# Performance work log

Measured on AMD Instinct MI355X. Metric: run time of the kernel, lower is better.

## Reference

```python
import jax, jax.numpy as jnp
import numpy as np

REG_WEIGHT = 1e-4
N_LAYERS = 3


def setup_inputs() -> dict:
    key = jax.random.key(0)
    ks = jax.random.split(key, 7)
    n_users, n_items, d = 100000, 50000, 64
    E, B = 1600000, 4096
    return {
        "user_table": jax.random.normal(ks[0], (n_users, d), dtype=jnp.float32) * 0.01,
        "item_table": jax.random.normal(ks[1], (n_items, d), dtype=jnp.float32) * 0.01,
        "edge_u": jax.random.randint(ks[2], (E,), 0, n_users, dtype=jnp.int32),
        "edge_i": jax.random.randint(ks[3], (E,), 0, n_items, dtype=jnp.int32),
        "users": jax.random.randint(ks[4], (B,), 0, n_users, dtype=jnp.int32),
        "pos_items": jax.random.randint(ks[5], (B,), 0, n_items, dtype=jnp.int32),
        "neg_items": jax.random.randint(ks[6], (B,), 0, n_items, dtype=jnp.int32),
    }


def _lightgcn_embeddings(user_table, item_table, edge_u, edge_i):
    n_users, n_items = user_table.shape[0], item_table.shape[0]
    N = n_users + n_items
    E = edge_u.shape[0]
    ones = jnp.ones((E,), dtype=user_table.dtype)
    # symmetric normalization D^{-1/2} A D^{-1/2} on the bipartite graph
    deg_u = jax.ops.segment_sum(ones, edge_u, num_segments=n_users)
    deg_i = jax.ops.segment_sum(ones, edge_i, num_segments=n_items)
    w = jax.lax.rsqrt(jnp.maximum(deg_u[edge_u] * deg_i[edge_i], 1.0))
    # symmetric edge list over the stacked [users; items] node set
    rows = jnp.concatenate([edge_u, edge_i + n_users])
    cols = jnp.concatenate([edge_i + n_users, edge_u])
    vals = jnp.concatenate([w, w])[:, None]

    x = jnp.concatenate([user_table, item_table], axis=0)  # [N, d]
    acc = x
    for _ in range(N_LAYERS):
        x = jax.ops.segment_sum(x[cols] * vals, rows, num_segments=N)
        acc = acc + x
    final = acc / jnp.asarray(N_LAYERS + 1, dtype=x.dtype)
    return final[:n_users], final[n_users:]


def reference(user_table, item_table, edge_u, edge_i, users, pos_items, neg_items):
    user_emb_all, item_emb_all = _lightgcn_embeddings(user_table, item_table, edge_u, edge_i)
    u_emb = user_emb_all[users]
    pos_i_emb = item_emb_all[pos_items]
    neg_i_emb = item_emb_all[neg_items]
    pos_scores = jnp.sum(u_emb * pos_i_emb, axis=-1)
    neg_scores = jnp.sum(u_emb * neg_i_emb, axis=-1)
    # L2 regularization on the layer-0 (table) embeddings
    u0 = user_table[users]
    p0 = item_table[pos_items]
    n0 = item_table[neg_items]
    reg_loss = REG_WEIGHT * (jnp.sum(u0 * u0) + jnp.sum(p0 * p0) + jnp.sum(n0 * n0))
    reg_loss = reg_loss / users.shape[0]
    return pos_scores, neg_scores, reg_loss
```

## Files before the change

kernel.cpp:

```cpp
#include <hip/hip_runtime.h>
#include <hip/hip_fp16.h>

#define THREADS 256
#define BIN_C 4096
#define NBMAX 400
#define CAP 4608
#define SH_U 8
#define SH_I 7
#define CPAD 16
#define T_TILES 8
#define TSH_U 13
#define TSH_I 14

__global__ void bin_kernel(const int* __restrict__ eu, const int* __restrict__ ei,
                           int* __restrict__ bcnt_u, int* __restrict__ bcnt_i,
                           int* __restrict__ binu, int* __restrict__ bini,
                           int E, int nbu, int nbi) {
    __shared__ int hist_u[NBMAX], hist_i[NBMAX];
    __shared__ int base_u[NBMAX], base_i[NBMAX];
    int tid = threadIdx.x;
    int e0 = blockIdx.x * BIN_C;
    if (e0 >= E) return;
    int cnt = min(BIN_C, E - e0);

    for (int b = tid; b < NBMAX; b += THREADS) { hist_u[b] = 0; hist_i[b] = 0; }
    __syncthreads();

    int u[16], v[16];
    #pragma unroll
    for (int j = 0; j < 16; ++j) {
        int k = tid + j * THREADS;
        if (k < cnt) { u[j] = eu[e0 + k]; v[j] = ei[e0 + k]; }
        else         { u[j] = -1; v[j] = -1; }
    }
    #pragma unroll
    for (int j = 0; j < 16; ++j) {
        if (u[j] >= 0) {
            atomicAdd(&hist_u[u[j] >> SH_U], 1);
            atomicAdd(&hist_i[v[j] >> SH_I], 1);
        }
    }
    __syncthreads();
    for (int b = tid; b < NBMAX; b += THREADS) {
        int cu = hist_u[b], ci = hist_i[b];
        base_u[b] = (cu > 0 && b < nbu) ? atomicAdd(&bcnt_u[(size_t)b * CPAD], cu) : 0;
        base_i[b] = (ci > 0 && b < nbi) ? atomicAdd(&bcnt_i[(size_t)b * CPAD], ci) : 0;
        hist_u[b] = 0; hist_i[b] = 0;
    }
    __syncthreads();
    #pragma unroll
    for (int j = 0; j < 16; ++j) {
        if (u[j] >= 0) {
            int bu = u[j] >> SH_U;
            int pu = base_u[bu] + atomicAdd(&hist_u[bu], 1);
            if (pu < CAP) binu[(size_t)bu * CAP + pu] = ((u[j] & 255) << 16) | v[j];
            int bi = v[j] >> SH_I;
            int pi = base_i[bi] + atomicAdd(&hist_i[bi], 1);
            if (pi < CAP) bini[(size_t)bi * CAP + pi] = ((v[j] & 127) << 17) | u[j];
        }
    }
}

__global__ void place(const int* __restrict__ bcnt_u, const int* __restrict__ bcnt_i,
                      const int* __restrict__ binu, const int* __restrict__ bini,
                      int* __restrict__ offu, int* __restrict__ offi,
                      int* __restrict__ du, int* __restrict__ di,
                      float* __restrict__ rsdu, float* __restrict__ rsdi,
                      int* __restrict__ entu, int* __restrict__ enti,
                      int* __restrict__ curs,
                      int nbu, int nU, int nI) {
    __shared__ int stash[CAP];
    __shared__ int bin_cnt[THREADS * T_TILES];
    __shared__ int node_base[THREADS];
    __shared__ int wsum[4];
    __shared__ int bob_sh;
    int b = blockIdx.x;
    bool isU = (b < nbu);
    const int* bin; int base_node, nn, count;
    int *off, *deg, *ent; float* rsd;
    int losh, tsh, lomask;
    if (isU) {
        bin = binu + (size_t)b * CAP;
        base_node = b << SH_U; nn = min(256, nU - base_node);
        count = min(bcnt_u[(size_t)b * CPAD], CAP);
        off = offu; deg = du; rsd = rsdu; ent = entu;
        losh = 16; tsh = TSH_U; lomask = 0xFFFF;
    } else {
        int b2 = b - nbu;
        bin = bini + (size_t)b2 * CAP;
        base_node = b2 << SH_I; nn = min(128, nI - base_node);
        count = min(bcnt_i[(size_t)b2 * CPAD], CAP);
        off = offi; deg = di; rsd = rsdi; ent = enti;
        losh = 17; tsh = TSH_I; lomask = 0x1FFFF;
    }
    int tid = threadIdx.x;
    #pragma unroll
    for (int t = 0; t < T_TILES; ++t) bin_cnt[tid + t * THREADS] = 0;
    __syncthreads();
    for (int k = tid; k < count; k += THREADS) {
        int p = bin[k];
        stash[k] = p;
        int key = ((p >> losh) << 3) | ((p & lomask) >> tsh);
        atomicAdd(&bin_cnt[key], 1);
    }
    __syncthreads();
    int c = 0;
    {
        int base = tid * T_TILES;
        #pragma unroll
        for (int t = 0; t < T_TILES; ++t) {
            int v = bin_cnt[base + t];
            bin_cnt[base + t] = c;
            c += v;
        }
    }
    int seg = (c + 15) & ~15;
    int lane = tid & 63, wid = tid >> 6;
    int inc = seg;
    #pragma unroll
    for (int ofs = 1; ofs < 64; ofs <<= 1) {
        int t = __shfl_up(inc, ofs);
        if (lane >= ofs) inc += t;
    }
    if (lane == 63) wsum[wid] = inc;
    __syncthreads();
    int wofs = 0;
    #pragma unroll
    for (int w = 0; w < 4; ++w) wofs += (w < wid) ? wsum[w] : 0;
    int incl = inc + wofs;
    int excl = incl - seg;
    if (tid == THREADS - 1) bob_sh = atomicAdd(&curs[isU ? 0 : 1], incl);
    __syncthreads();
    int bob = bob_sh;
    node_base[tid] = excl;
    if (tid < nn) {
        off[base_node + tid] = bob + excl;
        deg[base_node + tid] = c;
        rsd[base_node + tid] = rsqrtf(fmaxf((float)c, 1.0f));
    }
    __syncthreads();
    #pragma unroll
    for (int t = 0; t < T_TILES; ++t) {
        int k = tid + t * THREADS;
        bin_cnt[k] += node_base[k >> 3];
    }
    __syncthreads();
    for (int k = tid; k < count; k += THREADS) {
        int p = stash[k];
        int key = ((p >> losh) << 3) | ((p & lomask) >> tsh);
        int sl = atomicAdd(&bin_cnt[key], 1);
        ent[bob + sl] = p & lomask;
    }
}

__global__ void conv16all(const float* __restrict__ ut, const float* __restrict__ it,
                          __half* __restrict__ dst, int nU16, int ntot16) {
    int stride = gridDim.x * blockDim.x;
    for (int i = blockIdx.x * blockDim.x + threadIdx.x; i < ntot16; i += stride) {
        const float* src = (i < nU16) ? (ut + (size_t)i * 4) : (it + (size_t)(i - nU16) * 4);
        float4 v = *reinterpret_cast<const float4*>(src);
        __half2 h0 = __float22half2_rn(make_float2(v.x, v.y));
        __half2 h1 = __float22half2_rn(make_float2(v.z, v.w));
        uint2 st;
        st.x = *reinterpret_cast<unsigned*>(&h0);
        st.y = *reinterpret_cast<unsigned*>(&h1);
        *reinterpret_cast<uint2*>(dst + (size_t)i * 4) = st;
    }
}

__global__ void prop16(const __half* __restrict__ x,
                       const int* __restrict__ offu, const int* __restrict__ offi,
                       const int* __restrict__ du, const int* __restrict__ di,
                       const float* __restrict__ rsdu, const float* __restrict__ rsdi,
                       const int* __restrict__ entu, const int* __restrict__ enti,
                       __half* __restrict__ y, int nU, int N) {
    int node = blockIdx.x * (THREADS >> 3) + (threadIdx.x >> 3);
    int lane = threadIdx.x & 7;
    if (node >= N) return;
    const int* ent; const __half* src; const float* rsdn;
    int beg, dg; float rs;
    if (node < nU) {
        beg = offu[node]; dg = du[node]; rs = rsdu[node];
        ent = entu; src = x + ((size_t)nU << 6); rsdn = rsdi;
    } else {
        int i = node - nU;
        beg = offi[i]; dg = di[i]; rs = rsdi[i];
        ent = enti; src = x; rsdn = rsdu;
    }
    float a0=0,a1=0,a2=0,a3=0,a4=0,a5=0,a6=0,a7=0;
    for (int k0 = 0; k0 < dg; k0 += 8) {
        int me = (k0 + lane < dg) ? ent[beg + k0 + lane] : 0;
        #pragma unroll
        for (int j = 0; j < 8; ++j) {
            if (k0 + j < dg) {
                int nbr = __shfl(me, j, 8);
                float w = rsdn[nbr];
                uint4 r = *reinterpret_cast<const uint4*>(src + ((size_t)nbr << 6) + (lane << 3));
                __half2 h0 = *reinterpret_cast<__half2*>(&r.x);
                __half2 h1 = *reinterpret_cast<__half2*>(&r.y);
                __half2 h2 = *reinterpret_cast<__half2*>(&r.z);
                __half2 h3 = *reinterpret_cast<__half2*>(&r.w);
                float2 f0 = __half22float2(h0), f1 = __half22float2(h1);
                float2 f2 = __half22float2(h2), f3 = __half22float2(h3);
                a0 += w * f0.x; a1 += w * f0.y; a2 += w * f1.x; a3 += w * f1.y;
                a4 += w * f2.x; a5 += w * f2.y; a6 += w * f3.x; a7 += w * f3.y;
            }
        }
    }
    __half2 o0 = __float22half2_rn(make_float2(a0 * rs, a1 * rs));
    __half2 o1 = __float22half2_rn(make_float2(a2 * rs, a3 * rs));
    __half2 o2 = __float22half2_rn(make_float2(a4 * rs, a5 * rs));
    __half2 o3 = __float22half2_rn(make_float2(a6 * rs, a7 * rs));
    uint4 st;
    st.x = *reinterpret_cast<unsigned*>(&o0);
    st.y = *reinterpret_cast<unsigned*>(&o1);
    st.z = *reinterpret_cast<unsigned*>(&o2);
    st.w = *reinterpret_cast<unsigned*>(&o3);
    *reinterpret_cast<uint4*>(y + ((size_t)node << 6) + (lane << 3)) = st;
}

__global__ void prop_sel_acc(const __half* __restrict__ x,
                             const int* __restrict__ users, const int* __restrict__ pos,
                             const int* __restrict__ neg,
                             const int* __restrict__ offu, const int* __restrict__ offi,
                             const int* __restrict__ du, const int* __restrict__ di,
                             const float* __restrict__ rsdu, const float* __restrict__ rsdi,
                             const int* __restrict__ entu, const int* __restrict__ enti,
                             float* __restrict__ sel, int B, int nU) {
    int r = blockIdx.x * (THREADS >> 3) + (threadIdx.x >> 3);
    int lane = threadIdx.x & 7;
    if (r >= 3 * B) return;
    int which = r / B, b = r - which * B;
    const int* ent; const __half* src; const float* rsdn;
    int beg, dg; float rs; size_t selfrow;
    if (which == 0) {
        int u = users[b];
        beg = offu[u]; dg = du[u]; rs = rsdu[u];
        ent = entu; src = x + ((size_t)nU << 6); rsdn = rsdi;
        selfrow = (size_t)u << 6;
    } else {
        int i = (which == 1) ? pos[b] : neg[b];
        beg = offi[i]; dg = di[i]; rs = rsdi[i];
        ent = enti; src = x; rsdn = rsdu;
        selfrow = (size_t)(nU + i) << 6;
    }
    float a0=0,a1=0,a2=0,a3=0,a4=0,a5=0,a6=0,a7=0;
    for (int k0 = 0; k0 < dg; k0 += 8) {
        int me = (k0 + lane < dg) ? ent[beg + k0 + lane] : 0;
        #pragma unroll
        for (int j = 0; j < 8; ++j) {
            if (k0 + j < dg) {
                int nbr = __shfl(me, j, 8);
                float w = rsdn[nbr];
                uint4 rv = *reinterpret_cast<const uint4*>(src + ((size_t)nbr << 6) + (lane << 3));
                __half2 h0 = *reinterpret_cast<__half2*>(&rv.x);
                __half2 h1 = *reinterpret_cast<__half2*>(&rv.y);
                __half2 h2 = *reinterpret_cast<__half2*>(&rv.z);
                __half2 h3 = *reinterpret_cast<__half2*>(&rv.w);
                float2 f0 = __half22float2(h0), f1 = __half22float2(h1);
                float2 f2 = __half22float2(h2), f3 = __half22float2(h3);
                a0 += w * f0.x; a1 += w * f0.y; a2 += w * f1.x; a3 += w * f1.y;
                a4 += w * f2.x; a5 += w * f2.y; a6 += w * f3.x; a7 += w * f3.y;
            }
        }
    }
    uint4 rv = *reinterpret_cast<const uint4*>(x + selfrow + (lane << 3));
    __half2 h0 = *reinterpret_cast<__half2*>(&rv.x);
    __half2 h1 = *reinterpret_cast<__half2*>(&rv.y);
    __half2 h2 = *reinterpret_cast<__half2*>(&rv.z);
    __half2 h3 = *reinterpret_cast<__half2*>(&rv.w);
    float2 s0 = __half22float2(h0), s1 = __half22float2(h1);
    float2 s2 = __half22float2(h2), s3 = __half22float2(h3);
    float* s = sel + ((size_t)r << 6) + (lane << 3);
    float4 d0 = *reinterpret_cast<float4*>(s);
    float4 d1 = *reinterpret_cast<float4*>(s + 4);
    d0.x += s0.x + rs * a0; d0.y += s0.y + rs * a1;
    d0.z += s1.x + rs * a2; d0.w += s1.y + rs * a3;
    d1.x += s2.x + rs * a4; d1.y += s2.y + rs * a5;
    d1.z += s3.x + rs * a6; d1.w += s3.y + rs * a7;
    *reinterpret_cast<float4*>(s) = d0;
    *reinterpret_cast<float4*>(s + 4) = d1;
}

__global__ void selreg(const float* __restrict__ ut, const float* __restrict__ it,
                       const int* __restrict__ users, const int* __restrict__ pos,
                       const int* __restrict__ neg,
                       float* __restrict__ sel, float* __restrict__ out_reg,
                       int B, float scale) {
    int r = blockIdx.x * (THREADS >> 4) + (threadIdx.x >> 4);
    int t = threadIdx.x & 15;
    float ssq = 0.f;
    if (r < 3 * B) {
        int which = r / B, b = r - which * B;
        const float* base; int idx;
        if (which == 0)      { base = ut; idx = users[b]; }
        else if (which == 1) { base = it; idx = pos[b]; }
        else                 { base = it; idx = neg[b]; }
        float4 v = *reinterpret_cast<const float4*>(base + ((size_t)idx << 6) + t * 4);
        *reinterpret_cast<float4*>(sel + ((size_t)r << 6) + t * 4) = v;
        ssq = v.x * v.x + v.y * v.y + v.z * v.z + v.w * v.w;
    }
    #pragma unroll
    for (int ofs = 32; ofs; ofs >>= 1) ssq += __shfl_down(ssq, ofs);
    if ((threadIdx.x & 63) == 0) atomicAdd(out_reg, ssq * scale);
}

__global__ void sel_acc16(const __half* __restrict__ x,
                          const int* __restrict__ users, const int* __restrict__ pos,
                          const int* __restrict__ neg, float* __restrict__ sel, int B, int nU) {
    int r = blockIdx.x * (THREADS >> 3) + (threadIdx.x >> 3);
    int lane = threadIdx.x & 7;
    if (r >= 3 * B) return;
    int which = r / B, b = r - which * B;
    size_t row;
    if (which == 0)      row = (size_t)users[b];
    else if (which == 1) row = (size_t)nU + pos[b];
    else                 row = (size_t)nU + neg[b];
    uint4 rv = *reinterpret_cast<const uint4*>(x + (row << 6) + (lane << 3));
    __half2 h0 = *reinterpret_cast<__half2*>(&rv.x);
    __half2 h1 = *reinterpret_cast<__half2*>(&rv.y);
    __half2 h2 = *reinterpret_cast<__half2*>(&rv.z);
    __half2 h3 = *reinterpret_cast<__half2*>(&rv.w);
    float2 f0 = __half22float2(h0), f1 = __half22float2(h1);
    float2 f2 = __half22float2(h2), f3 = __half22float2(h3);
    float* s = sel + ((size_t)r << 6) + (lane << 3);
    float4 d0 = *reinterpret_cast<float4*>(s);
    float4 d1 = *reinterpret_cast<float4*>(s + 4);
    d0.x += f0.x; d0.y += f0.y; d0.z += f1.x; d0.w += f1.y;
    d1.x += f2.x; d1.y += f2.y; d1.z += f3.x; d1.w += f3.y;
    *reinterpret_cast<float4*>(s) = d0;
    *reinterpret_cast<float4*>(s + 4) = d1;
}

__global__ void score(const float* __restrict__ sel, float* __restrict__ out, int B) {
    int b = blockIdx.x * (THREADS >> 6) + (threadIdx.x >> 6);
    int lane = threadIdx.x & 63;
    if (b >= B) return;
    float u = sel[((size_t)b << 6) + lane];
    float p = sel[((size_t)(B + b) << 6) + lane];
    float n = sel[((size_t)(2 * B + b) << 6) + lane];
    float ps = u * p, ns = u * n;
    for (int ofs = 32; ofs; ofs >>= 1) {
        ps += __shfl_down(ps, ofs);
        ns += __shfl_down(ns, ofs);
    }
    if (lane == 0) {
        out[b]     = ps * (1.0f / 16.0f);
        out[B + b] = ns * (1.0f / 16.0f);
    }
}

extern "C" void kernel_launch(void* const* d_in, const int* in_sizes, int n_in,
                              void* d_out, int out_size, void* d_ws, size_t ws_size,
                              hipStream_t stream) {
    const float* ut   = (const float*)d_in[0];
    const float* it   = (const float*)d_in[1];
    const int* eu     = (const int*)d_in[2];
    const int* ei     = (const int*)d_in[3];
    const int* users  = (const int*)d_in[4];
    const int* pos    = (const int*)d_in[5];
    const int* neg    = (const int*)d_in[6];
    int nU = in_sizes[0] / 64;
    int nI = in_sizes[1] / 64;
    int E  = in_sizes[2];
    int B  = in_sizes[4];
    int N  = nU + nI;
    float* out = (float*)d_out;

    int nbu = (nU + 255) >> SH_U;
    int nbi = (nI + 127) >> SH_I;

    char* ws = (char*)d_ws;
    size_t cursor = 0;
    auto alloc = [&](size_t bytes) -> void* {
        cursor = (cursor + 255) & ~(size_t)255;
        void* p = ws + cursor;
        cursor += bytes;
        return p;
    };
    int*   bcnt_u = (int*)alloc((size_t)nbu * CPAD * 4);
    int*   bcnt_i = (int*)alloc((size_t)nbi * CPAD * 4);
    int*   curs   = (int*)alloc(2 * 4);
    size_t zero_span = cursor;
    int*   binu = (int*)alloc((size_t)nbu * CAP * 4);
    int*   bini = (int*)alloc((size_t)nbi * CAP * 4);
    int*   offu = (int*)alloc((size_t)nU * 4);
    int*   offi = (int*)alloc((size_t)nI * 4);
    int*   du   = (int*)alloc((size_t)nU * 4);
    int*   di   = (int*)alloc((size_t)nI * 4);
    float* rsdu = (float*)alloc((size_t)nU * 4);
    float* rsdi = (float*)alloc((size_t)nI * 4);
    int*   entu = (int*)alloc(((size_t)E + (size_t)nbu * 256 * 16) * 4);
    int*   enti = (int*)alloc(((size_t)E + (size_t)nbi * 128 * 16) * 4);
    __half* xA  = (__half*)alloc((size_t)N * 64 * 2);
    __half* xB  = (__half*)alloc((size_t)N * 64 * 2);
    float* sel  = (float*)alloc((size_t)3 * B * 64 * 4);

    hipMemsetAsync(d_ws, 0, zero_span, stream);
    hipMemsetAsync(out + 2 * B, 0, sizeof(float), stream);

    conv16all<<<2048, THREADS, 0, stream>>>(ut, it, xA, nU * 16, N * 16);

    int nchunks = (E + BIN_C - 1) / BIN_C;
    bin_kernel<<<nchunks, THREADS, 0, stream>>>(eu, ei, bcnt_u, bcnt_i, binu, bini, E, nbu, nbi);
    place<<<nbu + nbi, THREADS, 0, stream>>>(bcnt_u, bcnt_i, binu, bini,
                                             offu, offi, du, di, rsdu, rsdi, entu, enti,
                                             curs, nbu, nU, nI);

    selreg<<<(3 * B + 15) / 16, THREADS, 0, stream>>>(ut, it, users, pos, neg, sel,
                                                      out + 2 * B, B, 1e-4f / (float)B);

    int gridSel16 = (3 * B * 8 + THREADS - 1) / THREADS;
    int gridProp = (N * 8 + THREADS - 1) / THREADS;
    prop16<<<gridProp, THREADS, 0, stream>>>(xA, offu, offi, du, di, rsdu, rsdi, entu, enti, xB, nU, N);
    sel_acc16<<<gridSel16, THREADS, 0, stream>>>(xB, users, pos, neg, sel, B, nU);
    prop16<<<gridProp, THREADS, 0, stream>>>(xB, offu, offi, du, di, rsdu, rsdi, entu, enti, xA, nU, N);
    prop_sel_acc<<<gridSel16, THREADS, 0, stream>>>(xA, users, pos, neg, offu, offi, du, di,
                                                    rsdu, rsdi, entu, enti, sel, B, nU);

    score<<<(B + 3) / 4, THREADS, 0, stream>>>(sel, out, B);
}
```

Baseline: 284.7 us.

## Replace global-atomic edge binning with per-chunk local sort and offset tables

The binning kernel no longer reserves space in global per-bin counters with atomics. Each chunk now sorts its edges by bin into its own contiguous region and writes a per-chunk prefix table. The place kernel then gathers each bin's slices from every chunk via these tables. This removes contended global atomics and scattered writes, but place now reads about 391 small segments per bin with serial per-thread loops and uneven lengths.

```diff
diff --git a/kernel.cpp b/kernel.cpp
--- a/kernel.cpp
+++ b/kernel.cpp
@@ -2,8 +2,8 @@
 #include <hip/hip_fp16.h>
 
 #define THREADS 256
-#define BIN_C 4096
-#define NBMAX 400
+#define BIN_C2 4096
+#define NBMAX 392
 #define CAP 4608
 #define SH_U 8
 #define SH_I 7
@@ -12,94 +12,117 @@
 #define TSH_U 13
 #define TSH_I 14
 
-__global__ void bin_kernel(const int* __restrict__ eu, const int* __restrict__ ei,
-                           int* __restrict__ bcnt_u, int* __restrict__ bcnt_i,
-                           int* __restrict__ binu, int* __restrict__ bini,
-                           int E, int nbu, int nbi) {
-    __shared__ int hist_u[NBMAX], hist_i[NBMAX];
-    __shared__ int base_u[NBMAX], base_i[NBMAX];
+__global__ void binpack(const int* __restrict__ eu, const int* __restrict__ ei,
+                        int* __restrict__ regu, int* __restrict__ regi,
+                        int* __restrict__ sTu, int* __restrict__ sTi,
+                        int E, int nbu, int nbi) {
+    int c = blockIdx.x;
+    bool isU = (blockIdx.y == 0);
+    const int* key   = isU ? eu : ei;
+    const int* other = isU ? ei : eu;
+    int nb   = isU ? nbu : nbi;
+    int sh   = isU ? SH_U : SH_I;
+    int losh = isU ? 16 : 17;
+    int lomsk = (1 << sh) - 1;
+    int* reg = isU ? regu : regi;
+    int* sT  = (isU ? sTu : sTi) + (size_t)c * (NBMAX);
+    __shared__ int hist[NBMAX];
+    __shared__ int wsum[4];
     int tid = threadIdx.x;
-    int e0 = blockIdx.x * BIN_C;
-    if (e0 >= E) return;
-    int cnt = min(BIN_C, E - e0);
-
-    for (int b = tid; b < NBMAX; b += THREADS) { hist_u[b] = 0; hist_i[b] = 0; }
-    __syncthreads();
-
-    int u[16], v[16];
-    #pragma unroll
-    for (int j = 0; j < 16; ++j) {
-        int k = tid + j * THREADS;
-        if (k < cnt) { u[j] = eu[e0 + k]; v[j] = ei[e0 + k]; }
-        else         { u[j] = -1; v[j] = -1; }
-    }
-    #pragma unroll
-    for (int j = 0; j < 16; ++j) {
-        if (u[j] >= 0) {
-            atomicAdd(&hist_u[u[j] >> SH_U], 1);
-            atomicAdd(&hist_i[v[j] >> SH_I], 1);
-        }
-    }
-    __syncthreads();
-    for (int b = tid; b < NBMAX; b += THREADS) {
-        int cu = hist_u[b], ci = hist_i[b];
-        base_u[b] = (cu > 0 && b < nbu) ? atomicAdd(&bcnt_u[(size_t)b * CPAD], cu) : 0;
-        base_i[b] = (ci > 0 && b < nbi) ? atomicAdd(&bcnt_i[(size_t)b * CPAD], ci) : 0;
-        hist_u[b] = 0; hist_i[b] = 0;
-    }
-    __syncthreads();
-    #pragma unroll
-    for (int j = 0; j < 16; ++j) {
-        if (u[j] >= 0) {
-            int bu = u[j] >> SH_U;
-            int pu = base_u[bu] + atomicAdd(&hist_u[bu], 1);
-            if (pu < CAP) binu[(size_t)bu * CAP + pu] = ((u[j] & 255) << 16) | v[j];
-            int bi = v[j] >> SH_I;
-            int pi = base_i[bi] + atomicAdd(&hist_i[bi], 1);
-            if (pi < CAP) bini[(size_t)bi * CAP + pi] = ((v[j] & 127) << 17) | u[j];
-        }
-    }
-}
-
-__global__ void place(const int* __restrict__ bcnt_u, const int* __restrict__ bcnt_i,
-                      const int* __restrict__ binu, const int* __restrict__ bini,
+    int e0 = c * BIN_C2;
+    int cnt = min(BIN_C2, E - e0);
+    if (cnt <= 0) return;
+    for (int b = tid; b < nb; b += THREADS) hist[b] = 0;
+    __syncthreads();
+    for (int k = tid; k < cnt; k += THREADS)
+        atomicAdd(&hist[key[e0 + k] >> sh], 1);
+    __syncthreads();
+    int b0 = tid * 2;
+    int v0 = (b0 < nb)     ? hist[b0]     : 0;
+    int v1 = (b0 + 1 < nb) ? hist[b0 + 1] : 0;
+    int s2 = v0 + v1;
+    int lane = tid & 63, wid = tid >> 6;
+    int inc = s2;
+    #pragma unroll
+    for (int ofs = 1; ofs < 64; ofs <<= 1) {
+        int t = __shfl_up(inc, ofs);
+        if (lane >= ofs) inc += t;
+    }
+    if (lane == 63) wsum[wid] = inc;
+    __syncthreads();
+    int wofs = 0;
+    #pragma unroll
+    for (int w = 0; w < 4; ++w) wofs += (w < wid) ? wsum[w] : 0;
+    int excl = inc - s2 + wofs;
+    __syncthreads();
+    if (b0 < nb)     { hist[b0] = excl;          sT[b0] = excl; }
+    if (b0 + 1 < nb) { hist[b0 + 1] = excl + v0; sT[b0 + 1] = excl + v0; }
+    if (tid == THREADS - 1) sT[nb] = cnt;
+    __syncthreads();
+    for (int k = tid; k < cnt; k += THREADS) {
+        int kn = key[e0 + k];
+        int o  = other[e0 + k];
+        int b  = kn >> sh;
+        int p  = ((kn & lomsk) << losh) | o;
+        int pos = atomicAdd(&hist[b], 1);
+        reg[(size_t)c * BIN_C2 + pos] = p;
+    }
+}
+
+__global__ void place(const int* __restrict__ regu, const int* __restrict__ regi,
+                      const int* __restrict__ sTu, const int* __restrict__ sTi,
                       int* __restrict__ offu, int* __restrict__ offi,
                       int* __restrict__ du, int* __restrict__ di,
                       float* __restrict__ rsdu, float* __restrict__ rsdi,
                       int* __restrict__ entu, int* __restrict__ enti,
                       int* __restrict__ curs,
-                      int nbu, int nU, int nI) {
+                      int nbu, int nU, int nI, int nchunks) {
     __shared__ int stash[CAP];
     __shared__ int bin_cnt[THREADS * T_TILES];
     __shared__ int node_base[THREADS];
     __shared__ int wsum[4];
     __shared__ int bob_sh;
+    __shared__ int scursor;
     int b = blockIdx.x;
     bool isU = (b < nbu);
-    const int* bin; int base_node, nn, count;
+    int bidx = isU ? b : (b - nbu);
+    const int* reg = isU ? regu : regi;
+    const int* sT  = isU ? sTu : sTi;
+    int base_node, nn;
     int *off, *deg, *ent; float* rsd;
-    int losh, tsh, lomask;
+    int losh, tsh;
     if (isU) {
-        bin = binu + (size_t)b * CAP;
-        base_node = b << SH_U; nn = min(256, nU - base_node);
-        count = min(bcnt_u[(size_t)b * CPAD], CAP);
+        base_node = bidx << SH_U; nn = min(256, nU - base_node);
         off = offu; deg = du; rsd = rsdu; ent = entu;
-        losh = 16; tsh = TSH_U; lomask = 0xFFFF;
+        losh = 16; tsh = TSH_U;
     } else {
-        int b2 = b - nbu;
-        bin = bini + (size_t)b2 * CAP;
-        base_node = b2 << SH_I; nn = min(128, nI - base_node);
-        count = min(bcnt_i[(size_t)b2 * CPAD], CAP);
+        base_node = bidx << SH_I; nn = min(128, nI - base_node);
         off = offi; deg = di; rsd = rsdi; ent = enti;
-        losh = 17; tsh = TSH_I; lomask = 0x1FFFF;
-    }
+        losh = 17; tsh = TSH_I;
+    }
+    int lomask = (1 << losh) - 1;
     int tid = threadIdx.x;
+    if (tid == 0) scursor = 0;
     #pragma unroll
     for (int t = 0; t < T_TILES; ++t) bin_cnt[tid + t * THREADS] = 0;
     __syncthreads();
+    for (int c = tid; c < nchunks; c += THREADS) {
+        const int* row = sT + (size_t)c * NBMAX;
+        int s = row[bidx], e = row[bidx + 1];
+        int len = e - s;
+        if (len > 0) {
+            int base = atomicAdd(&scursor, len);
+            const int* src = reg + (size_t)c * BIN_C2 + s;
+            for (int j = 0; j < len; ++j) {
+                int pos = base + j;
+                if (pos < CAP) stash[pos] = src[j];
+            }
+        }
+    }
+    __syncthreads();
+    int count = min(scursor, CAP);
     for (int k = tid; k < count; k += THREADS) {
-        int p = bin[k];
-        stash[k] = p;
+        int p = stash[k];
         int key = ((p >> losh) << 3) | ((p & lomask) >> tsh);
         atomicAdd(&bin_cnt[key], 1);
     }
@@ -129,7 +152,7 @@
     for (int w = 0; w < 4; ++w) wofs += (w < wid) ? wsum[w] : 0;
     int incl = inc + wofs;
     int excl = incl - seg;
-    if (tid == THREADS - 1) bob_sh = atomicAdd(&curs[isU ? 0 : 1], incl);
+    if (tid == THREADS - 1) bob_sh = atomicAdd(&curs[isU ? 0 : CPAD], incl);
     __syncthreads();
     int bob = bob_sh;
     node_base[tid] = excl;
@@ -369,6 +392,7 @@
 
     int nbu = (nU + 255) >> SH_U;
     int nbi = (nI + 127) >> SH_I;
+    int nchunks = (E + BIN_C2 - 1) / BIN_C2;
 
     char* ws = (char*)d_ws;
     size_t cursor = 0;
@@ -378,12 +402,12 @@
         cursor += bytes;
         return p;
     };
-    int*   bcnt_u = (int*)alloc((size_t)nbu * CPAD * 4);
-    int*   bcnt_i = (int*)alloc((size_t)nbi * CPAD * 4);
-    int*   curs   = (int*)alloc(2 * 4);
+    int*   curs = (int*)alloc(2 * CPAD * 4);
     size_t zero_span = cursor;
-    int*   binu = (int*)alloc((size_t)nbu * CAP * 4);
-    int*   bini = (int*)alloc((size_t)nbi * CAP * 4);
+    int*   regu = (int*)alloc((size_t)nchunks * BIN_C2 * 4);
+    int*   regi = (int*)alloc((size_t)nchunks * BIN_C2 * 4);
+    int*   sTu  = (int*)alloc((size_t)nchunks * NBMAX * 4);
+    int*   sTi  = (int*)alloc((size_t)nchunks * NBMAX * 4);
     int*   offu = (int*)alloc((size_t)nU * 4);
     int*   offi = (int*)alloc((size_t)nI * 4);
     int*   du   = (int*)alloc((size_t)nU * 4);
@@ -401,11 +425,10 @@
 
     conv16all<<<2048, THREADS, 0, stream>>>(ut, it, xA, nU * 16, N * 16);
 
-    int nchunks = (E + BIN_C - 1) / BIN_C;
-    bin_kernel<<<nchunks, THREADS, 0, stream>>>(eu, ei, bcnt_u, bcnt_i, binu, bini, E, nbu, nbi);
-    place<<<nbu + nbi, THREADS, 0, stream>>>(bcnt_u, bcnt_i, binu, bini,
+    binpack<<<dim3(nchunks, 2), THREADS, 0, stream>>>(eu, ei, regu, regi, sTu, sTi, E, nbu, nbi);
+    place<<<nbu + nbi, THREADS, 0, stream>>>(regu, regi, sTu, sTi,
                                              offu, offi, du, di, rsdu, rsdi, entu, enti,
-                                             curs, nbu, nU, nI);
+                                             curs, nbu, nU, nI, nchunks);
 
     selreg<<<(3 * B + 15) / 16, THREADS, 0, stream>>>(ut, it, users, pos, neg, sel,
                                                       out + 2 * B, B, 1e-4f / (float)B);
```

Result: no change. 280.6 us (-1.4%).

## Merge independent kernels into multi-role launches and add nontemporal edge loads/stores

Applied to the files above, without the earlier changes.

Merges the fp16 conversion, edge binning and selection/regularization kernels into one launch that picks its role from blockIdx.y. It also folds the first layer's selection accumulation into the second propagation launch as extra blocks. Together these cut the launch count and let independent work overlap. Edge-list loads and propagation output stores now use nontemporal hints, and the place cursors are padded apart to avoid sharing a cache line. The risks are oversized grids with many idle blocks and poorer cache reuse of the nontemporal output, which the next layer reads back.

```diff
diff --git a/kernel.cpp b/kernel.cpp
--- a/kernel.cpp
+++ b/kernel.cpp
@@ -12,20 +12,61 @@
 #define TSH_U 13
 #define TSH_I 14
 
-__global__ void bin_kernel(const int* __restrict__ eu, const int* __restrict__ ei,
-                           int* __restrict__ bcnt_u, int* __restrict__ bcnt_i,
-                           int* __restrict__ binu, int* __restrict__ bini,
-                           int E, int nbu, int nbi) {
+typedef unsigned u32x4 __attribute__((ext_vector_type(4)));
+
+__global__ void megaA(const float* __restrict__ ut, const float* __restrict__ it,
+                      __half* __restrict__ dst, int nU16, int ntot16,
+                      const int* __restrict__ eu, const int* __restrict__ ei,
+                      int* __restrict__ bcnt_u, int* __restrict__ bcnt_i,
+                      int* __restrict__ binu, int* __restrict__ bini,
+                      int E, int nbu, int nbi, int nchunks,
+                      const int* __restrict__ users, const int* __restrict__ pos,
+                      const int* __restrict__ neg,
+                      float* __restrict__ sel, float* __restrict__ out_reg,
+                      int B, float scale) {
+    int tid = threadIdx.x;
+    if (blockIdx.y == 0) {
+        int stride = gridDim.x * blockDim.x;
+        for (int i = blockIdx.x * blockDim.x + tid; i < ntot16; i += stride) {
+            const float* src = (i < nU16) ? (ut + (size_t)i * 4) : (it + (size_t)(i - nU16) * 4);
+            float4 v = *reinterpret_cast<const float4*>(src);
+            __half2 h0 = __float22half2_rn(make_float2(v.x, v.y));
+            __half2 h1 = __float22half2_rn(make_float2(v.z, v.w));
+            uint2 st;
+            st.x = *reinterpret_cast<unsigned*>(&h0);
+            st.y = *reinterpret_cast<unsigned*>(&h1);
+            *reinterpret_cast<uint2*>(dst + (size_t)i * 4) = st;
+        }
+        return;
+    }
+    if (blockIdx.y == 2) {
+        int r = blockIdx.x * (THREADS >> 4) + (tid >> 4);
+        int t = tid & 15;
+        float ssq = 0.f;
+        if (r < 3 * B) {
+            int which = r / B, b = r - which * B;
+            const float* base; int idx;
+            if (which == 0)      { base = ut; idx = users[b]; }
+            else if (which == 1) { base = it; idx = pos[b]; }
+            else                 { base = it; idx = neg[b]; }
+            float4 v = *reinterpret_cast<const float4*>(base + ((size_t)idx << 6) + t * 4);
+            *reinterpret_cast<float4*>(sel + ((size_t)r << 6) + t * 4) = v;
+            ssq = v.x * v.x + v.y * v.y + v.z * v.z + v.w * v.w;
+        }
+        #pragma unroll
+        for (int ofs = 32; ofs; ofs >>= 1) ssq += __shfl_down(ssq, ofs);
+        if ((tid & 63) == 0) atomicAdd(out_reg, ssq * scale);
+        return;
+    }
     __shared__ int hist_u[NBMAX], hist_i[NBMAX];
     __shared__ int base_u[NBMAX], base_i[NBMAX];
-    int tid = threadIdx.x;
-    int e0 = blockIdx.x * BIN_C;
-    if (e0 >= E) return;
+    int c = blockIdx.x;
+    if (c >= nchunks) return;
+    int e0 = c * BIN_C;
     int cnt = min(BIN_C, E - e0);
-
+    if (cnt <= 0) return;
     for (int b = tid; b < NBMAX; b += THREADS) { hist_u[b] = 0; hist_i[b] = 0; }
     __syncthreads();
-
     int u[16], v[16];
     #pragma unroll
     for (int j = 0; j < 16; ++j) {
@@ -78,21 +119,22 @@
     bool isU = (b < nbu);
     const int* bin; int base_node, nn, count;
     int *off, *deg, *ent; float* rsd;
-    int losh, tsh, lomask;
+    int losh, tsh;
     if (isU) {
         bin = binu + (size_t)b * CAP;
         base_node = b << SH_U; nn = min(256, nU - base_node);
         count = min(bcnt_u[(size_t)b * CPAD], CAP);
         off = offu; deg = du; rsd = rsdu; ent = entu;
-        losh = 16; tsh = TSH_U; lomask = 0xFFFF;
+        losh = 16; tsh = TSH_U;
     } else {
         int b2 = b - nbu;
         bin = bini + (size_t)b2 * CAP;
         base_node = b2 << SH_I; nn = min(128, nI - base_node);
         count = min(bcnt_i[(size_t)b2 * CPAD], CAP);
         off = offi; deg = di; rsd = rsdi; ent = enti;
-        losh = 17; tsh = TSH_I; lomask = 0x1FFFF;
-    }
+        losh = 17; tsh = TSH_I;
+    }
+    int lomask = (1 << losh) - 1;
     int tid = threadIdx.x;
     #pragma unroll
     for (int t = 0; t < T_TILES; ++t) bin_cnt[tid + t * THREADS] = 0;
@@ -129,7 +171,7 @@
     for (int w = 0; w < 4; ++w) wofs += (w < wid) ? wsum[w] : 0;
     int incl = inc + wofs;
     int excl = incl - seg;
-    if (tid == THREADS - 1) bob_sh = atomicAdd(&curs[isU ? 0 : 1], incl);
+    if (tid == THREADS - 1) bob_sh = atomicAdd(&curs[isU ? 0 : CPAD], incl);
     __syncthreads();
     int bob = bob_sh;
     node_base[tid] = excl;
@@ -153,29 +195,12 @@
     }
 }
 
-__global__ void conv16all(const float* __restrict__ ut, const float* __restrict__ it,
-                          __half* __restrict__ dst, int nU16, int ntot16) {
-    int stride = gridDim.x * blockDim.x;
-    for (int i = blockIdx.x * blockDim.x + threadIdx.x; i < ntot16; i += stride) {
-        const float* src = (i < nU16) ? (ut + (size_t)i * 4) : (it + (size_t)(i - nU16) * 4);
-        float4 v = *reinterpret_cast<const float4*>(src);
-        __half2 h0 = __float22half2_rn(make_float2(v.x, v.y));
-        __half2 h1 = __float22half2_rn(make_float2(v.z, v.w));
-        uint2 st;
-        st.x = *reinterpret_cast<unsigned*>(&h0);
-        st.y = *reinterpret_cast<unsigned*>(&h1);
-        *reinterpret_cast<uint2*>(dst + (size_t)i * 4) = st;
-    }
-}
-
-__global__ void prop16(const __half* __restrict__ x,
-                       const int* __restrict__ offu, const int* __restrict__ offi,
-                       const int* __restrict__ du, const int* __restrict__ di,
-                       const float* __restrict__ rsdu, const float* __restrict__ rsdi,
-                       const int* __restrict__ entu, const int* __restrict__ enti,
-                       __half* __restrict__ y, int nU, int N) {
-    int node = blockIdx.x * (THREADS >> 3) + (threadIdx.x >> 3);
-    int lane = threadIdx.x & 7;
+__device__ __forceinline__ void prop_body(const __half* __restrict__ x,
+                                          const int* __restrict__ offu, const int* __restrict__ offi,
+                                          const int* __restrict__ du, const int* __restrict__ di,
+                                          const float* __restrict__ rsdu, const float* __restrict__ rsdi,
+                                          const int* __restrict__ entu, const int* __restrict__ enti,
+                                          __half* __restrict__ y, int nU, int N, int node, int lane) {
     if (node >= N) return;
     const int* ent; const __half* src; const float* rsdn;
     int beg, dg; float rs;
@@ -189,7 +214,7 @@
     }
     float a0=0,a1=0,a2=0,a3=0,a4=0,a5=0,a6=0,a7=0;
     for (int k0 = 0; k0 < dg; k0 += 8) {
-        int me = (k0 + lane < dg) ? ent[beg + k0 + lane] : 0;
+        int me = (k0 + lane < dg) ? __builtin_nontemporal_load(&ent[beg + k0 + lane]) : 0;
         #pragma unroll
         for (int j = 0; j < 8; ++j) {
             if (k0 + j < dg) {
@@ -211,12 +236,59 @@
     __half2 o1 = __float22half2_rn(make_float2(a2 * rs, a3 * rs));
     __half2 o2 = __float22half2_rn(make_float2(a4 * rs, a5 * rs));
     __half2 o3 = __float22half2_rn(make_float2(a6 * rs, a7 * rs));
-    uint4 st;
+    u32x4 st;
     st.x = *reinterpret_cast<unsigned*>(&o0);
     st.y = *reinterpret_cast<unsigned*>(&o1);
     st.z = *reinterpret_cast<unsigned*>(&o2);
     st.w = *reinterpret_cast<unsigned*>(&o3);
-    *reinterpret_cast<uint4*>(y + ((size_t)node << 6) + (lane << 3)) = st;
+    __builtin_nontemporal_store(st, reinterpret_cast<u32x4*>(y + ((size_t)node << 6) + (lane << 3)));
+}
+
+__global__ void prop16(const __half* __restrict__ x,
+                       const int* __restrict__ offu, const int* __restrict__ offi,
+                       const int* __restrict__ du, const int* __restrict__ di,
+                       const float* __restrict__ rsdu, const float* __restrict__ rsdi,
+                       const int* __restrict__ entu, const int* __restrict__ enti,
+                       __half* __restrict__ y, int nU, int N) {
+    int node = blockIdx.x * (THREADS >> 3) + (threadIdx.x >> 3);
+    prop_body(x, offu, offi, du, di, rsdu, rsdi, entu, enti, y, nU, N, node, threadIdx.x & 7);
+}
+
+__global__ void prop16_selacc(const __half* __restrict__ x,
+                              const int* __restrict__ offu, const int* __restrict__ offi,
+                              const int* __restrict__ du, const int* __restrict__ di,
+                              const float* __restrict__ rsdu, const float* __restrict__ rsdi,
+                              const int* __restrict__ entu, const int* __restrict__ enti,
+                              __half* __restrict__ y, int nU, int N, int gridProp,
+                              const int* __restrict__ users, const int* __restrict__ pos,
+                              const int* __restrict__ neg, float* __restrict__ sel, int B) {
+    int lane = threadIdx.x & 7;
+    if (blockIdx.x < gridProp) {
+        int node = blockIdx.x * (THREADS >> 3) + (threadIdx.x >> 3);
+        prop_body(x, offu, offi, du, di, rsdu, rsdi, entu, enti, y, nU, N, node, lane);
+        return;
+    }
+    int r = (blockIdx.x - gridProp) * (THREADS >> 3) + (threadIdx.x >> 3);
+    if (r >= 3 * B) return;
+    int which = r / B, b = r - which * B;
+    size_t row;
+    if (which == 0)      row = (size_t)users[b];
+    else if (which == 1) row = (size_t)nU + pos[b];
+    else                 row = (size_t)nU + neg[b];
+    uint4 rv = *reinterpret_cast<const uint4*>(x + (row << 6) + (lane << 3));
+    __half2 h0 = *reinterpret_cast<__half2*>(&rv.x);
+    __half2 h1 = *reinterpret_cast<__half2*>(&rv.y);
+    __half2 h2 = *reinterpret_cast<__half2*>(&rv.z);
+    __half2 h3 = *reinterpret_cast<__half2*>(&rv.w);
+    float2 f0 = __half22float2(h0), f1 = __half22float2(h1);
+    float2 f2 = __half22float2(h2), f3 = __half22float2(h3);
+    float* s = sel + ((size_t)r << 6) + (lane << 3);
+    float4 d0 = *reinterpret_cast<float4*>(s);
+    float4 d1 = *reinterpret_cast<float4*>(s + 4);
+    d0.x += f0.x; d0.y += f0.y; d0.z += f1.x; d0.w += f1.y;
+    d1.x += f2.x; d1.y += f2.y; d1.z += f3.x; d1.w += f3.y;
+    *reinterpret_cast<float4*>(s) = d0;
+    *reinterpret_cast<float4*>(s + 4) = d1;
 }
 
 __global__ void prop_sel_acc(const __half* __restrict__ x,
@@ -246,7 +318,7 @@
     }
     float a0=0,a1=0,a2=0,a3=0,a4=0,a5=0,a6=0,a7=0;
     for (int k0 = 0; k0 < dg; k0 += 8) {
-        int me = (k0 + lane < dg) ? ent[beg + k0 + lane] : 0;
+        int me = (k0 + lane < dg) ? __builtin_nontemporal_load(&ent[beg + k0 + lane]) : 0;
         #pragma unroll
         for (int j = 0; j < 8; ++j) {
             if (k0 + j < dg) {
@@ -282,56 +354,6 @@
     *reinterpret_cast<float4*>(s + 4) = d1;
 }
 
-__global__ void selreg(const float* __restrict__ ut, const float* __restrict__ it,
-                       const int* __restrict__ users, const int* __restrict__ pos,
-                       const int* __restrict__ neg,
-                       float* __restrict__ sel, float* __restrict__ out_reg,
-                       int B, float scale) {
-    int r = blockIdx.x * (THREADS >> 4) + (threadIdx.x >> 4);
-    int t = threadIdx.x & 15;
-    float ssq = 0.f;
-    if (r < 3 * B) {
-        int which = r / B, b = r - which * B;
-        const float* base; int idx;
-        if (which == 0)      { base = ut; idx = users[b]; }
-        else if (which == 1) { base = it; idx = pos[b]; }
-        else                 { base = it; idx = neg[b]; }
-        float4 v = *reinterpret_cast<const float4*>(base + ((size_t)idx << 6) + t * 4);
-        *reinterpret_cast<float4*>(sel + ((size_t)r << 6) + t * 4) = v;
-        ssq = v.x * v.x + v.y * v.y + v.z * v.z + v.w * v.w;
-    }
-    #pragma unroll
-    for (int ofs = 32; ofs; ofs >>= 1) ssq += __shfl_down(ssq, ofs);
-    if ((threadIdx.x & 63) == 0) atomicAdd(out_reg, ssq * scale);
-}
-
-__global__ void sel_acc16(const __half* __restrict__ x,
-                          const int* __restrict__ users, const int* __restrict__ pos,
-                          const int* __restrict__ neg, float* __restrict__ sel, int B, int nU) {
-    int r = blockIdx.x * (THREADS >> 3) + (threadIdx.x >> 3);
-    int lane = threadIdx.x & 7;
-    if (r >= 3 * B) return;
-    int which = r / B, b = r - which * B;
-    size_t row;
-    if (which == 0)      row = (size_t)users[b];
-    else if (which == 1) row = (size_t)nU + pos[b];
-    else                 row = (size_t)nU + neg[b];
-    uint4 rv = *reinterpret_cast<const uint4*>(x + (row << 6) + (lane << 3));
-    __half2 h0 = *reinterpret_cast<__half2*>(&rv.x);
-    __half2 h1 = *reinterpret_cast<__half2*>(&rv.y);
-    __half2 h2 = *reinterpret_cast<__half2*>(&rv.z);
-    __half2 h3 = *reinterpret_cast<__half2*>(&rv.w);
-    float2 f0 = __half22float2(h0), f1 = __half22float2(h1);
-    float2 f2 = __half22float2(h2), f3 = __half22float2(h3);
-    float* s = sel + ((size_t)r << 6) + (lane << 3);
-    float4 d0 = *reinterpret_cast<float4*>(s);
-    float4 d1 = *reinterpret_cast<float4*>(s + 4);
-    d0.x += f0.x; d0.y += f0.y; d0.z += f1.x; d0.w += f1.y;
-    d1.x += f2.x; d1.y += f2.y; d1.z += f3.x; d1.w += f3.y;
-    *reinterpret_cast<float4*>(s) = d0;
-    *reinterpret_cast<float4*>(s + 4) = d1;
-}
-
 __global__ void score(const float* __restrict__ sel, float* __restrict__ out, int B) {
     int b = blockIdx.x * (THREADS >> 6) + (threadIdx.x >> 6);
     int lane = threadIdx.x & 63;
@@ -369,6 +391,7 @@
 
     int nbu = (nU + 255) >> SH_U;
     int nbi = (nI + 127) >> SH_I;
+    int nchunks = (E + BIN_C - 1) / BIN_C;
 
     char* ws = (char*)d_ws;
     size_t cursor = 0;
@@ -380,7 +403,7 @@
     };
     int*   bcnt_u = (int*)alloc((size_t)nbu * CPAD * 4);
     int*   bcnt_i = (int*)alloc((size_t)nbi * CPAD * 4);
-    int*   curs   = (int*)alloc(2 * 4);
+    int*   curs   = (int*)alloc(2 * CPAD * 4);
     size_t zero_span = cursor;
     int*   binu = (int*)alloc((size_t)nbu * CAP * 4);
     int*   bini = (int*)alloc((size_t)nbi * CAP * 4);
@@ -399,22 +422,25 @@
     hipMemsetAsync(d_ws, 0, zero_span, stream);
     hipMemsetAsync(out + 2 * B, 0, sizeof(float), stream);
 
-    conv16all<<<2048, THREADS, 0, stream>>>(ut, it, xA, nU * 16, N * 16);
-
-    int nchunks = (E + BIN_C - 1) / BIN_C;
-    bin_kernel<<<nchunks, THREADS, 0, stream>>>(eu, ei, bcnt_u, bcnt_i, binu, bini, E, nbu, nbi);
+    int gax = max(nchunks, max(1024, (3 * B + 15) / 16));
+    megaA<<<dim3(gax, 3), THREADS, 0, stream>>>(ut, it, xA, nU * 16, N * 16,
+                                                eu, ei, bcnt_u, bcnt_i, binu, bini,
+                                                E, nbu, nbi, nchunks,
+                                                users, pos, neg, sel, out + 2 * B,
+                                                B, 1e-4f / (float)B);
+
     place<<<nbu + nbi, THREADS, 0, stream>>>(bcnt_u, bcnt_i, binu, bini,
                                              offu, offi, du, di, rsdu, rsdi, entu, enti,
                                              curs, nbu, nU, nI);
 
-    selreg<<<(3 * B + 15) / 16, THREADS, 0, stream>>>(ut, it, users, pos, neg, sel,
-                                                      out + 2 * B, B, 1e-4f / (float)B);
-
     int gridSel16 = (3 * B * 8 + THREADS - 1) / THREADS;
     int gridProp = (N * 8 + THREADS - 1) / THREADS;
     prop16<<<gridProp, THREADS, 0, stream>>>(xA, offu, offi, du, di, rsdu, rsdi, entu, enti, xB, nU, N);
-    sel_acc16<<<gridSel16, THREADS, 0, stream>>>(xB, users, pos, neg, sel, B, nU);
-    prop16<<<gridProp, THREADS, 0, stream>>>(xB, offu, offi, du, di, rsdu, rsdi, entu, enti, xA, nU, N);
+
+    prop16_selacc<<<gridProp + gridSel16, THREADS, 0, stream>>>(
+        xB, offu, offi, du, di, rsdu, rsdi, entu, enti, xA, nU, N, gridProp,
+        users, pos, neg, sel, B);
+
     prop_sel_acc<<<gridSel16, THREADS, 0, stream>>>(xA, users, pos, neg, offu, offi, du, di,
                                                     rsdu, rsdi, entu, enti, sel, B, nU);
 
```

Measured after the change: 282.8 us. Within noise of the previous version (-0.7%).
